# Performance work log

Hardware: AMD Instinct MI355X
Metric: run time of the kernel (lower is better)

Reference implementation:

```python
import jax, jax.numpy as jnp
import numpy as np

D_MODEL = 128; N_HEADS = 8; N_LEVELS = 1; N_POINTS = 8
MAX_RES = 10.0
B, H_SP, W_SP = 8, 64, 64


def setup_inputs() -> dict:
    key = jax.random.key(0)
    ks = jax.random.split(key, 8)
    s = 0.02
    f32 = jnp.float32
    return {
        "nbr_fea": jax.random.normal(ks[0], (B, D_MODEL, H_SP, W_SP), f32),
        "ext_fea": jax.random.normal(ks[1], (B, D_MODEL, H_SP, W_SP), f32),
        "W_val": jax.random.normal(ks[2], (D_MODEL, D_MODEL), f32) * s,
        "b_val": jnp.zeros((D_MODEL,), f32),
        "W_off": jax.random.normal(ks[3], (D_MODEL, N_HEADS * N_LEVELS * N_POINTS * 2), f32) * s,
        "b_off": jax.random.normal(ks[4], (N_HEADS * N_LEVELS * N_POINTS * 2,), f32) * s,
        "W_attn": jax.random.normal(ks[5], (D_MODEL, N_HEADS * N_LEVELS * N_POINTS), f32) * s,
        "b_attn": jnp.zeros((N_HEADS * N_LEVELS * N_POINTS,), f32),
        "W_out": jax.random.normal(ks[6], (D_MODEL, D_MODEL), f32) * s,
        "b_out": jnp.zeros((D_MODEL,), f32),
    }


def _deform_attn_align(nbr_fea, ext_fea, W_val, b_val, W_off, b_off, W_attn, b_attn, W_out, b_out):
    b, c, h, w = nbr_fea.shape
    L = h * w
    dh = c // N_HEADS
    # flatten b c h w -> b (h w) c
    query = jnp.transpose(ext_fea, (0, 2, 3, 1)).reshape(b, L, c)
    vin = jnp.transpose(nbr_fea, (0, 2, 3, 1)).reshape(b, L, c)

    # value projection (mask is all-False -> no masked fill needed)
    value = (vin @ W_val + b_val).reshape(b, L, N_HEADS, dh)
    vh = jnp.transpose(value, (0, 2, 1, 3))  # [b, H, L, dh]

    # sampling offsets, clamped by max_residue_magnitude * tanh
    off = MAX_RES * jnp.tanh(query @ W_off + b_off)
    off = off.reshape(b, L, N_HEADS, N_POINTS, 2)  # single level
    attn = jax.nn.softmax((query @ W_attn + b_attn).reshape(b, L, N_HEADS, N_POINTS), axis=-1)

    # reference points in [0,1]; valid_ratio == 1 since padding mask is all-False
    yy, xx = jnp.meshgrid(jnp.arange(h, dtype=jnp.float32), jnp.arange(w, dtype=jnp.float32), indexing="ij")
    ref = jnp.stack([(xx.reshape(-1) + 0.5) / w, (yy.reshape(-1) + 0.5) / h], axis=-1)  # [L, 2]
    norm = jnp.array([w, h], jnp.float32)  # offset_normalizer [W, H]
    loc = ref[None, :, None, None, :] + off / norm  # [b, L, H, P, 2]

    # grid_sample(align_corners=False, padding_mode='zeros') pixel coordinates
    px = jnp.transpose(loc[..., 0] * w - 0.5, (0, 2, 1, 3))  # [b, H, L, P]
    py = jnp.transpose(loc[..., 1] * h - 0.5, (0, 2, 1, 3))

    x0 = jnp.floor(px); y0 = jnp.floor(py)
    fx = px - x0; fy = py - y0
    x0i = x0.astype(jnp.int32); y0i = y0.astype(jnp.int32)

    def gather(xi, yi):
        valid = (xi >= 0) & (xi < w) & (yi >= 0) & (yi < h)
        idx = jnp.clip(yi, 0, h - 1) * w + jnp.clip(xi, 0, w - 1)  # [b, H, L, P]
        g = jnp.take_along_axis(vh, idx.reshape(b, N_HEADS, L * N_POINTS)[..., None], axis=2)
        return g.reshape(b, N_HEADS, L, N_POINTS, dh) * valid[..., None]

    samp = (gather(x0i, y0i) * ((1.0 - fx) * (1.0 - fy))[..., None]
            + gather(x0i + 1, y0i) * (fx * (1.0 - fy))[..., None]
            + gather(x0i, y0i + 1) * ((1.0 - fx) * fy)[..., None]
            + gather(x0i + 1, y0i + 1) * (fx * fy)[..., None])  # [b, H, L, P, dh]

    aw = jnp.transpose(attn, (0, 2, 1, 3))  # [b, H, L, P]
    out = jnp.sum(samp * aw[..., None], axis=3)  # [b, H, L, dh]
    out = jnp.transpose(out, (0, 2, 1, 3)).reshape(b, L, c)
    out = out @ W_out + b_out
    return jnp.transpose(out.reshape(b, h, w, c), (0, 3, 1, 2))  # b c h w


def reference(nbr_fea, ext_fea, W_val, b_val, W_off, b_off, W_attn, b_attn, W_out, b_out):
    return _deform_attn_align(nbr_fea, ext_fea, W_val, b_val, W_off, b_off, W_attn, b_attn, W_out, b_out)
```

## Files before the change

kernel.cpp:

```cpp
#include <hip/hip_runtime.h>
#include <cstdint>

#define HB 8
#define CM 128
#define NHEAD 8
#define NPT 8
#define DHD 16
#define HS 64
#define WS 64
#define LTOT 4096
#define NQA 192

typedef float floatx4 __attribute__((ext_vector_type(4)));
typedef short bf16x8 __attribute__((ext_vector_type(8)));

__device__ __forceinline__ unsigned short f2bf_rne(float x) {
  unsigned u = __float_as_uint(x);
  return (unsigned short)((u + 0x7FFFu + ((u >> 16) & 1)) >> 16);
}
__device__ __forceinline__ void split_bf(float x, unsigned short& h, unsigned short& l) {
  unsigned u = __float_as_uint(x);
  h = (unsigned short)(u >> 16);
  float r = x - __uint_as_float(u & 0xFFFF0000u);
  l = (unsigned short)(__float_as_uint(r) >> 16);
}
__device__ __forceinline__ float fast_tanh(float x) {
  float e = __expf(2.0f * x);
  return 1.0f - 2.0f / (e + 1.0f);
}

__global__ __launch_bounds__(256) void prep(const float* __restrict__ Wv,
                                            const float* __restrict__ Wo,
                                            const float* __restrict__ Wa,
                                            const float* __restrict__ Ww,
                                            const float* __restrict__ bo,
                                            const float* __restrict__ ba,
                                            unsigned short* __restrict__ wf_val,
                                            unsigned short* __restrict__ wf_qa,
                                            unsigned short* __restrict__ wf_out,
                                            float* __restrict__ bias_qa) {
  const int gid = blockIdx.x * 256 + threadIdx.x;
  const int k4 = gid / 448;
  const int ng = gid - k4 * 448;

  const float* src;
  unsigned short* dst;
  int Nsrc, Nn, nd, n;
  if (ng < 128) {        src = Wv; dst = wf_val; Nsrc = 128; Nn = 128; n = ng;        nd = n; }
  else if (ng < 256) {   src = Wo; dst = wf_qa;  Nsrc = 128; Nn = 192; n = ng - 128;  nd = n; }
  else if (ng < 320) {   src = Wa; dst = wf_qa;  Nsrc = 64;  Nn = 192; n = ng - 256;  nd = n + 128; }
  else {                 src = Ww; dst = wf_out; Nsrc = 128; Nn = 128; n = ng - 320;  nd = n; }

  ushort4 hi, lo;
  split_bf(src[(k4 * 4 + 0) * Nsrc + n], hi.x, lo.x);
  split_bf(src[(k4 * 4 + 1) * Nsrc + n], hi.y, lo.y);
  split_bf(src[(k4 * 4 + 2) * Nsrc + n], hi.z, lo.z);
  split_bf(src[(k4 * 4 + 3) * Nsrc + n], hi.w, lo.w);
  const int off = (k4 >> 1) * Nn * 8 + nd * 8 + (k4 & 1) * 4;
  *(ushort4*)(dst + off) = hi;
  *(ushort4*)(dst + Nn * 128 + off) = lo;

  if (gid < 128) bias_qa[gid] = bo[gid];
  else if (gid < 192) bias_qa[gid] = ba[gid - 128];
}

template <int N, int OUT_MODE>
__device__ __forceinline__ void gemm_wide(const float* __restrict__ A,
                                          const unsigned short* __restrict__ WF,
                                          const float* __restrict__ bias,
                                          void* __restrict__ outv,
                                          int b, int ml0, int t, char* smem) {
  constexpr int NT = N / 32;
  unsigned short* AB = (unsigned short*)smem;

  {
    const float* src = A + (size_t)b * CM * LTOT + ml0;
    const int x = t & 63, kq = t >> 6;
#pragma unroll
    for (int i = 0; i < 8; i++) {
      const int kb = kq * 4 + i * 16;
      ushort4 hi, lo;
      split_bf(src[(size_t)(kb + 0) * LTOT + x], hi.x, lo.x);
      split_bf(src[(size_t)(kb + 1) * LTOT + x], hi.y, lo.y);
      split_bf(src[(size_t)(kb + 2) * LTOT + x], hi.z, lo.z);
      split_bf(src[(size_t)(kb + 3) * LTOT + x], hi.w, lo.w);
      const int off = x * 128 + (((kb >> 3) ^ (x & 15)) << 3) + (kb & 7);
      *(ushort4*)(AB + off) = hi;
      *(ushort4*)(AB + 8192 + off) = lo;
    }
  }
  __syncthreads();

  const int w = t >> 6, lane = t & 63;
  const int wm = (w >> 1) * 32, wn = (w & 1) * (N / 2);
  const int nl = lane & 15, q = lane >> 4;

  floatx4 acc[2][NT];
#pragma unroll
  for (int mt = 0; mt < 2; mt++)
#pragma unroll
    for (int j = 0; j < NT; j++) acc[mt][j] = {0.0f, 0.0f, 0.0f, 0.0f};

#pragma unroll
  for (int K0 = 0; K0 < 4; K0++) {
    bf16x8 ah[2], al[2];
#pragma unroll
    for (int mt = 0; mt < 2; mt++) {
      const int m = wm + mt * 16 + nl;
      const int off = m * 128 + (((K0 * 4 + q) ^ (m & 15)) << 3);
      ah[mt] = *(bf16x8*)(AB + off);
      al[mt] = *(bf16x8*)(AB + 8192 + off);
    }
#pragma unroll
    for (int j = 0; j < NT; j++) {
      const int n = wn + j * 16 + nl;
      const size_t o = (size_t)(K0 * 4 + q) * N * 8 + n * 8;
      const bf16x8 wh = *(const bf16x8*)(WF + o);
      const bf16x8 wl = *(const bf16x8*)(WF + (size_t)N * 128 + o);
#pragma unroll
      for (int mt = 0; mt < 2; mt++) {
        acc[mt][j] = __builtin_amdgcn_mfma_f32_16x16x32_bf16(al[mt], wh, acc[mt][j], 0, 0, 0);
        acc[mt][j] = __builtin_amdgcn_mfma_f32_16x16x32_bf16(ah[mt], wl, acc[mt][j], 0, 0, 0);
        acc[mt][j] = __builtin_amdgcn_mfma_f32_16x16x32_bf16(ah[mt], wh, acc[mt][j], 0, 0, 0);
      }
    }
  }

#pragma unroll
  for (int j = 0; j < NT; j++) {
    const int gc = wn + j * 16 + nl;
    const float bv = bias[gc];
#pragma unroll
    for (int mt = 0; mt < 2; mt++)
#pragma unroll
      for (int r = 0; r < 4; r++) {
        const int m = ml0 + wm + mt * 16 + q * 4 + r;
        const float v = acc[mt][j][r] + bv;
        if (OUT_MODE == 0)
          ((unsigned short*)outv)[(((size_t)b * NHEAD + (gc >> 4)) * LTOT + m) * DHD + (gc & 15)] =
              f2bf_rne(v);
        else
          ((float*)outv)[((size_t)b * LTOT + m) * NQA + gc] = v;
      }
  }
}

__global__ __launch_bounds__(256, 4) void gemm_vq(const float* __restrict__ nbr,
                                                  const float* __restrict__ ext,
                                                  const unsigned short* __restrict__ wf_val,
                                                  const unsigned short* __restrict__ wf_qa,
                                                  const float* __restrict__ b_val,
                                                  const float* __restrict__ bias_qa,
                                                  unsigned short* __restrict__ value,
                                                  float* __restrict__ qa) {
  __shared__ char smem[32768];
  if (blockIdx.y == 0)
    gemm_wide<128, 0>(nbr, wf_val, b_val, value, blockIdx.z, blockIdx.x * 64, threadIdx.x, smem);
  else
    gemm_wide<192, 1>(ext, wf_qa, bias_qa, qa, blockIdx.z, blockIdx.x * 64, threadIdx.x, smem);
}

__global__ __launch_bounds__(512, 2) void samp_out(const unsigned short* __restrict__ value,
                                                   const float* __restrict__ qa,
                                                   const unsigned short* __restrict__ wf_out,
                                                   const float* __restrict__ b_out,
                                                   float* __restrict__ out) {
  __shared__ char smem[65536];
  float2* WXY = (float2*)smem;
  float* WA = (float*)(smem + 32768);
  unsigned short* FR = (unsigned short*)(smem + 49152);
  const int t = threadIdx.x;
  const int b = blockIdx.x & 7;
  const int tile = blockIdx.x >> 3;
  const int ml0 = tile * 64;

  {
    const int ll = t >> 3, h = t & 7;
    const int l = ml0 + ll;
    const float* qrow = qa + ((size_t)b * LTOT + l) * NQA;
    float4 of[4];
#pragma unroll
    for (int j = 0; j < 4; j++) of[j] = *(const float4*)(qrow + h * 16 + j * 4);
    const float4 lga = *(const float4*)(qrow + 128 + h * 8);
    const float4 lgb = *(const float4*)(qrow + 128 + h * 8 + 4);
    const float lg[8] = {lga.x, lga.y, lga.z, lga.w, lgb.x, lgb.y, lgb.z, lgb.w};
    float m = lg[0];
#pragma unroll
    for (int p = 1; p < 8; p++) m = fmaxf(m, lg[p]);
    float e[8], s = 0.0f;
#pragma unroll
    for (int p = 0; p < 8; p++) { e[p] = __expf(lg[p] - m); s += e[p]; }
    const float inv = 1.0f / s;
    const float xf = (float)(l & (WS - 1));
    const float yf = (float)(l >> 6);
#pragma unroll
    for (int p = 0; p < 8; p++) {
      const float ox = (p & 1) ? of[p >> 1].z : of[p >> 1].x;
      const float oy = (p & 1) ? of[p >> 1].w : of[p >> 1].y;
      WXY[p * 512 + t] = {xf + 10.0f * fast_tanh(ox), yf + 10.0f * fast_tanh(oy)};
      WA[p * 512 + t] = e[p] * inv;
    }
  }
  __syncthreads();

  const int d4 = t & 3;
  const int u = t >> 2;
#pragma unroll
  for (int ps = 0; ps < 4; ps++) {
    const int uu = ps * 128 + u;
    const int ll = uu >> 3;
    const int h = uu & 7;
    const unsigned short* vbb = value + ((size_t)(b * NHEAD + h) * LTOT) * DHD + d4 * 4;

    float4 o = {0.0f, 0.0f, 0.0f, 0.0f};
#pragma unroll
    for (int p = 0; p < 8; p++) {
      const float2 pxy = WXY[p * 512 + uu];
      const float aw = WA[p * 512 + uu];
      const float x0f = floorf(pxy.x), y0f = floorf(pxy.y);
      const float fx = pxy.x - x0f, fy = pxy.y - y0f;
      const int ix = (int)x0f, iy = (int)y0f;
#pragma unroll
      for (int c = 0; c < 4; c++) {
        const int cdx = c & 1, cdy = c >> 1;
        const int jx = ix + cdx, jy = iy + cdy;
        const float wx = cdx ? fx : 1.0f - fx;
        const float wy = cdy ? fy : 1.0f - fy;
        const bool valid = ((unsigned)jx < WS) & ((unsigned)jy < HS);
        const float wc = valid ? aw * wx * wy : 0.0f;
        const int cx = min(max(jx, 0), WS - 1);
        const int cy = min(max(jy, 0), HS - 1);
        const uint2 rw = *(const uint2*)(vbb + (size_t)((cy << 6) + cx) * DHD);
        o.x += wc * __uint_as_float(rw.x << 16);
        o.y += wc * __uint_as_float(rw.x & 0xFFFF0000u);
        o.z += wc * __uint_as_float(rw.y << 16);
        o.w += wc * __uint_as_float(rw.y & 0xFFFF0000u);
      }
    }

    const int off = ll * 128 + (((h * 2 + (d4 >> 1)) ^ (ll & 15)) << 3) + (d4 & 1) * 4;
    ushort4 st = {f2bf_rne(o.x), f2bf_rne(o.y), f2bf_rne(o.z), f2bf_rne(o.w)};
    *(ushort4*)(FR + off) = st;
  }
  __syncthreads();

  const int w = t >> 6, lane = t & 63;
  const int nl = lane & 15, q = lane >> 4;
  const int wm = (w >> 1) * 16;
  const int wn = (w & 1) * 64;

  floatx4 acc[4];
#pragma unroll
  for (int j = 0; j < 4; j++) acc[j] = {0.0f, 0.0f, 0.0f, 0.0f};

#pragma unroll
  for (int K0 = 0; K0 < 4; K0++) {
    const int m = wm + nl;
    const int off = m * 128 + (((K0 * 4 + q) ^ (m & 15)) << 3);
    const bf16x8 ah = *(bf16x8*)(FR + off);
#pragma unroll
    for (int j = 0; j < 4; j++) {
      const int n = wn + j * 16 + nl;
      const size_t o = (size_t)(K0 * 4 + q) * CM * 8 + n * 8;
      const bf16x8 wh = *(const bf16x8*)(wf_out + o);
      const bf16x8 wl = *(const bf16x8*)(wf_out + (size_t)CM * 128 + o);
      acc[j] = __builtin_amdgcn_mfma_f32_16x16x32_bf16(ah, wl, acc[j], 0, 0, 0);
      acc[j] = __builtin_amdgcn_mfma_f32_16x16x32_bf16(ah, wh, acc[j], 0, 0, 0);
    }
  }

  __syncthreads();
  float* LF = (float*)smem;
#pragma unroll
  for (int j = 0; j < 4; j++) {
    const int n = wn + j * 16 + nl;
#pragma unroll
    for (int r = 0; r < 4; r++) LF[n * 65 + wm + q * 4 + r] = acc[j][r];
  }
  __syncthreads();

#pragma unroll
  for (int i = 0; i < 16; i++) {
    const int idx = t + i * 512;
    const int n = idx >> 6, m = idx & 63;
    out[((size_t)b * CM + n) * LTOT + ml0 + m] = LF[n * 65 + m] + b_out[n];
  }
}

extern "C" void kernel_launch(void* const* d_in, const int* in_sizes, int n_in,
                              void* d_out, int out_size, void* d_ws, size_t ws_size,
                              hipStream_t stream) {
  const float* nbr    = (const float*)d_in[0];
  const float* ext    = (const float*)d_in[1];
  const float* W_val  = (const float*)d_in[2];
  const float* b_val  = (const float*)d_in[3];
  const float* W_off  = (const float*)d_in[4];
  const float* b_off  = (const float*)d_in[5];
  const float* W_attn = (const float*)d_in[6];
  const float* b_attn = (const float*)d_in[7];
  const float* W_out  = (const float*)d_in[8];
  const float* b_out  = (const float*)d_in[9];
  float* out = (float*)d_out;

  unsigned short* value = (unsigned short*)d_ws;
  float* qa = (float*)(value + (size_t)HB * NHEAD * LTOT * DHD);
  unsigned short* wf_val = (unsigned short*)(qa + (size_t)HB * LTOT * NQA);
  unsigned short* wf_qa  = wf_val + 128 * 128 * 2;
  unsigned short* wf_out = wf_qa + 192 * 128 * 2;
  float* bias_qa = (float*)(wf_out + 128 * 128 * 2);

  prep<<<56, 256, 0, stream>>>(W_val, W_off, W_attn, W_out, b_off, b_attn,
                               wf_val, wf_qa, wf_out, bias_qa);
  gemm_vq<<<dim3(64, 2, HB), 256, 0, stream>>>(nbr, ext, wf_val, wf_qa, b_val, bias_qa, value, qa);
  samp_out<<<dim3(512), 512, 0, stream>>>(value, qa, wf_out, b_out, out);
}
```

Measured before the change: 136.1 us.

## Fuse projection GEMMs, sampling and output GEMM into one persistent kernel with grid barrier

Merges the value/query GEMM kernel and the sampling+output kernel into a single 512-block kernel. Each block computes its value-projection tile, publishes it via an atomic counter, then computes the offset/attention projection straight into shared memory, so the qa intermediate never goes to global memory. It then spins on a grid-wide barrier before sampling value. This drops one kernel launch and the qa round-trip, but relies on all 512 blocks being co-resident to avoid deadlock and adds a spin-wait.

```diff
diff --git a/kernel.cpp b/kernel.cpp
--- a/kernel.cpp
+++ b/kernel.cpp
@@ -10,6 +10,8 @@
 #define WS 64
 #define LTOT 4096
 #define NQA 192
+#define QAP 196
+#define NBLK 512
 
 typedef float floatx4 __attribute__((ext_vector_type(4)));
 typedef short bf16x8 __attribute__((ext_vector_type(8)));
@@ -38,8 +40,10 @@
                                             unsigned short* __restrict__ wf_val,
                                             unsigned short* __restrict__ wf_qa,
                                             unsigned short* __restrict__ wf_out,
-                                            float* __restrict__ bias_qa) {
+                                            float* __restrict__ bias_qa,
+                                            unsigned int* __restrict__ bar) {
   const int gid = blockIdx.x * 256 + threadIdx.x;
+  if (gid == 0) *bar = 0;
   const int k4 = gid / 448;
   const int ng = gid - k4 * 448;
 
@@ -64,21 +68,37 @@
   else if (gid < 192) bias_qa[gid] = ba[gid - 128];
 }
 
-template <int N, int OUT_MODE>
-__device__ __forceinline__ void gemm_wide(const float* __restrict__ A,
-                                          const unsigned short* __restrict__ WF,
-                                          const float* __restrict__ bias,
-                                          void* __restrict__ outv,
-                                          int b, int ml0, int t, char* smem) {
-  constexpr int NT = N / 32;
+__global__ __launch_bounds__(512, 4) void fused(const float* __restrict__ nbr,
+                                                const float* __restrict__ ext,
+                                                const unsigned short* __restrict__ wf_val,
+                                                const unsigned short* __restrict__ wf_qa,
+                                                const unsigned short* __restrict__ wf_out,
+                                                const float* __restrict__ b_val,
+                                                const float* __restrict__ bias_qa,
+                                                const float* __restrict__ b_out,
+                                                unsigned short* __restrict__ value,
+                                                float* __restrict__ out,
+                                                unsigned int* __restrict__ bar) {
+  __shared__ char smem[65536];
   unsigned short* AB = (unsigned short*)smem;
-
-  {
-    const float* src = A + (size_t)b * CM * LTOT + ml0;
+  float* qaT = (float*)smem;
+  float2* WXY = (float2*)smem;
+  float* WA = (float*)(smem + 32768);
+  unsigned short* FR = (unsigned short*)(smem + 49152);
+  float* LF = (float*)smem;
+
+  const int t = threadIdx.x;
+  const int b = blockIdx.x & 7;
+  const int ml0 = (blockIdx.x >> 3) * 64;
+  const int wv = t >> 6, lane = t & 63;
+  const int nl = lane & 15, q = lane >> 4;
+
+  {
+    const float* src = nbr + (size_t)b * CM * LTOT + ml0;
     const int x = t & 63, kq = t >> 6;
 #pragma unroll
-    for (int i = 0; i < 8; i++) {
-      const int kb = kq * 4 + i * 16;
+    for (int i = 0; i < 4; i++) {
+      const int kb = i * 32 + kq * 4;
       ushort4 hi, lo;
       split_bf(src[(size_t)(kb + 0) * LTOT + x], hi.x, lo.x);
       split_bf(src[(size_t)(kb + 1) * LTOT + x], hi.y, lo.y);
@@ -91,98 +111,118 @@
   }
   __syncthreads();
 
-  const int w = t >> 6, lane = t & 63;
-  const int wm = (w >> 1) * 32, wn = (w & 1) * (N / 2);
-  const int nl = lane & 15, q = lane >> 4;
-
-  floatx4 acc[2][NT];
-#pragma unroll
-  for (int mt = 0; mt < 2; mt++)
-#pragma unroll
-    for (int j = 0; j < NT; j++) acc[mt][j] = {0.0f, 0.0f, 0.0f, 0.0f};
-
-#pragma unroll
-  for (int K0 = 0; K0 < 4; K0++) {
-    bf16x8 ah[2], al[2];
-#pragma unroll
-    for (int mt = 0; mt < 2; mt++) {
-      const int m = wm + mt * 16 + nl;
-      const int off = m * 128 + (((K0 * 4 + q) ^ (m & 15)) << 3);
-      ah[mt] = *(bf16x8*)(AB + off);
-      al[mt] = *(bf16x8*)(AB + 8192 + off);
-    }
-#pragma unroll
-    for (int j = 0; j < NT; j++) {
+  {
+    const int wn = wv * 16;
+    floatx4 acc[4];
+#pragma unroll
+    for (int mt = 0; mt < 4; mt++) acc[mt] = {0.0f, 0.0f, 0.0f, 0.0f};
+#pragma unroll
+    for (int K0 = 0; K0 < 4; K0++) {
+      bf16x8 ah[4], al[4];
+#pragma unroll
+      for (int mt = 0; mt < 4; mt++) {
+        const int off = (mt * 16 + nl) * 128 + (((K0 * 4 + q) ^ nl) << 3);
+        ah[mt] = *(bf16x8*)(AB + off);
+        al[mt] = *(bf16x8*)(AB + 8192 + off);
+      }
+      const size_t o = (size_t)(K0 * 4 + q) * CM * 8 + (wn + nl) * 8;
+      const bf16x8 wh = *(const bf16x8*)(wf_val + o);
+      const bf16x8 wl = *(const bf16x8*)(wf_val + (size_t)CM * 128 + o);
+#pragma unroll
+      for (int mt = 0; mt < 4; mt++) {
+        acc[mt] = __builtin_amdgcn_mfma_f32_16x16x32_bf16(al[mt], wh, acc[mt], 0, 0, 0);
+        acc[mt] = __builtin_amdgcn_mfma_f32_16x16x32_bf16(ah[mt], wl, acc[mt], 0, 0, 0);
+        acc[mt] = __builtin_amdgcn_mfma_f32_16x16x32_bf16(ah[mt], wh, acc[mt], 0, 0, 0);
+      }
+    }
+    const float bv = b_val[wn + nl];
+    unsigned short* vp = value + ((size_t)(b * NHEAD + wv) * LTOT) * DHD + nl;
+#pragma unroll
+    for (int mt = 0; mt < 4; mt++)
+#pragma unroll
+      for (int r = 0; r < 4; r++) {
+        const int m = ml0 + mt * 16 + q * 4 + r;
+        vp[(size_t)m * DHD] = f2bf_rne(acc[mt][r] + bv);
+      }
+  }
+  __syncthreads();
+
+  if (t == 0) {
+    __threadfence();
+    __hip_atomic_fetch_add(bar, 1u, __ATOMIC_RELEASE, __HIP_MEMORY_SCOPE_AGENT);
+  }
+
+  {
+    const float* src = ext + (size_t)b * CM * LTOT + ml0;
+    const int x = t & 63, kq = t >> 6;
+#pragma unroll
+    for (int i = 0; i < 4; i++) {
+      const int kb = i * 32 + kq * 4;
+      ushort4 hi, lo;
+      split_bf(src[(size_t)(kb + 0) * LTOT + x], hi.x, lo.x);
+      split_bf(src[(size_t)(kb + 1) * LTOT + x], hi.y, lo.y);
+      split_bf(src[(size_t)(kb + 2) * LTOT + x], hi.z, lo.z);
+      split_bf(src[(size_t)(kb + 3) * LTOT + x], hi.w, lo.w);
+      const int off = x * 128 + (((kb >> 3) ^ (x & 15)) << 3) + (kb & 7);
+      *(ushort4*)(AB + off) = hi;
+      *(ushort4*)(AB + 8192 + off) = lo;
+    }
+  }
+  __syncthreads();
+
+  {
+    const int wm = (wv >> 2) * 32;
+    const int wn = (wv & 3) * 48;
+    floatx4 acc[2][3];
+#pragma unroll
+    for (int mt = 0; mt < 2; mt++)
+#pragma unroll
+      for (int j = 0; j < 3; j++) acc[mt][j] = {0.0f, 0.0f, 0.0f, 0.0f};
+#pragma unroll
+    for (int K0 = 0; K0 < 4; K0++) {
+      bf16x8 ah[2], al[2];
+#pragma unroll
+      for (int mt = 0; mt < 2; mt++) {
+        const int off = (wm + mt * 16 + nl) * 128 + (((K0 * 4 + q) ^ nl) << 3);
+        ah[mt] = *(bf16x8*)(AB + off);
+        al[mt] = *(bf16x8*)(AB + 8192 + off);
+      }
+#pragma unroll
+      for (int j = 0; j < 3; j++) {
+        const size_t o = (size_t)(K0 * 4 + q) * NQA * 8 + (wn + j * 16 + nl) * 8;
+        const bf16x8 wh = *(const bf16x8*)(wf_qa + o);
+        const bf16x8 wl = *(const bf16x8*)(wf_qa + (size_t)NQA * 128 + o);
+#pragma unroll
+        for (int mt = 0; mt < 2; mt++) {
+          acc[mt][j] = __builtin_amdgcn_mfma_f32_16x16x32_bf16(al[mt], wh, acc[mt][j], 0, 0, 0);
+          acc[mt][j] = __builtin_amdgcn_mfma_f32_16x16x32_bf16(ah[mt], wl, acc[mt][j], 0, 0, 0);
+          acc[mt][j] = __builtin_amdgcn_mfma_f32_16x16x32_bf16(ah[mt], wh, acc[mt][j], 0, 0, 0);
+        }
+      }
+    }
+    __syncthreads();
+#pragma unroll
+    for (int j = 0; j < 3; j++) {
       const int n = wn + j * 16 + nl;
-      const size_t o = (size_t)(K0 * 4 + q) * N * 8 + n * 8;
-      const bf16x8 wh = *(const bf16x8*)(WF + o);
-      const bf16x8 wl = *(const bf16x8*)(WF + (size_t)N * 128 + o);
-#pragma unroll
-      for (int mt = 0; mt < 2; mt++) {
-        acc[mt][j] = __builtin_amdgcn_mfma_f32_16x16x32_bf16(al[mt], wh, acc[mt][j], 0, 0, 0);
-        acc[mt][j] = __builtin_amdgcn_mfma_f32_16x16x32_bf16(ah[mt], wl, acc[mt][j], 0, 0, 0);
-        acc[mt][j] = __builtin_amdgcn_mfma_f32_16x16x32_bf16(ah[mt], wh, acc[mt][j], 0, 0, 0);
-      }
-    }
-  }
-
-#pragma unroll
-  for (int j = 0; j < NT; j++) {
-    const int gc = wn + j * 16 + nl;
-    const float bv = bias[gc];
-#pragma unroll
-    for (int mt = 0; mt < 2; mt++)
-#pragma unroll
-      for (int r = 0; r < 4; r++) {
-        const int m = ml0 + wm + mt * 16 + q * 4 + r;
-        const float v = acc[mt][j][r] + bv;
-        if (OUT_MODE == 0)
-          ((unsigned short*)outv)[(((size_t)b * NHEAD + (gc >> 4)) * LTOT + m) * DHD + (gc & 15)] =
-              f2bf_rne(v);
-        else
-          ((float*)outv)[((size_t)b * LTOT + m) * NQA + gc] = v;
-      }
-  }
-}
-
-__global__ __launch_bounds__(256, 4) void gemm_vq(const float* __restrict__ nbr,
-                                                  const float* __restrict__ ext,
-                                                  const unsigned short* __restrict__ wf_val,
-                                                  const unsigned short* __restrict__ wf_qa,
-                                                  const float* __restrict__ b_val,
-                                                  const float* __restrict__ bias_qa,
-                                                  unsigned short* __restrict__ value,
-                                                  float* __restrict__ qa) {
-  __shared__ char smem[32768];
-  if (blockIdx.y == 0)
-    gemm_wide<128, 0>(nbr, wf_val, b_val, value, blockIdx.z, blockIdx.x * 64, threadIdx.x, smem);
-  else
-    gemm_wide<192, 1>(ext, wf_qa, bias_qa, qa, blockIdx.z, blockIdx.x * 64, threadIdx.x, smem);
-}
-
-__global__ __launch_bounds__(512, 2) void samp_out(const unsigned short* __restrict__ value,
-                                                   const float* __restrict__ qa,
-                                                   const unsigned short* __restrict__ wf_out,
-                                                   const float* __restrict__ b_out,
-                                                   float* __restrict__ out) {
-  __shared__ char smem[65536];
-  float2* WXY = (float2*)smem;
-  float* WA = (float*)(smem + 32768);
-  unsigned short* FR = (unsigned short*)(smem + 49152);
-  const int t = threadIdx.x;
-  const int b = blockIdx.x & 7;
-  const int tile = blockIdx.x >> 3;
-  const int ml0 = tile * 64;
+      const float bv = bias_qa[n];
+#pragma unroll
+      for (int mt = 0; mt < 2; mt++)
+#pragma unroll
+        for (int r = 0; r < 4; r++)
+          qaT[(wm + mt * 16 + q * 4 + r) * QAP + n] = acc[mt][j][r] + bv;
+    }
+  }
+  __syncthreads();
 
   {
     const int ll = t >> 3, h = t & 7;
-    const int l = ml0 + ll;
-    const float* qrow = qa + ((size_t)b * LTOT + l) * NQA;
+    const float* qrow = qaT + ll * QAP;
     float4 of[4];
 #pragma unroll
     for (int j = 0; j < 4; j++) of[j] = *(const float4*)(qrow + h * 16 + j * 4);
     const float4 lga = *(const float4*)(qrow + 128 + h * 8);
     const float4 lgb = *(const float4*)(qrow + 128 + h * 8 + 4);
+    __syncthreads();
     const float lg[8] = {lga.x, lga.y, lga.z, lga.w, lgb.x, lgb.y, lgb.z, lgb.w};
     float m = lg[0];
 #pragma unroll
@@ -191,6 +231,7 @@
 #pragma unroll
     for (int p = 0; p < 8; p++) { e[p] = __expf(lg[p] - m); s += e[p]; }
     const float inv = 1.0f / s;
+    const int l = ml0 + ll;
     const float xf = (float)(l & (WS - 1));
     const float yf = (float)(l >> 6);
 #pragma unroll
@@ -201,89 +242,91 @@
       WA[p * 512 + t] = e[p] * inv;
     }
   }
-  __syncthreads();
-
-  const int d4 = t & 3;
-  const int u = t >> 2;
-#pragma unroll
-  for (int ps = 0; ps < 4; ps++) {
-    const int uu = ps * 128 + u;
-    const int ll = uu >> 3;
-    const int h = uu & 7;
-    const unsigned short* vbb = value + ((size_t)(b * NHEAD + h) * LTOT) * DHD + d4 * 4;
-
-    float4 o = {0.0f, 0.0f, 0.0f, 0.0f};
-#pragma unroll
-    for (int p = 0; p < 8; p++) {
-      const float2 pxy = WXY[p * 512 + uu];
-      const float aw = WA[p * 512 + uu];
-      const float x0f = floorf(pxy.x), y0f = floorf(pxy.y);
-      const float fx = pxy.x - x0f, fy = pxy.y - y0f;
-      const int ix = (int)x0f, iy = (int)y0f;
-#pragma unroll
-      for (int c = 0; c < 4; c++) {
-        const int cdx = c & 1, cdy = c >> 1;
-        const int jx = ix + cdx, jy = iy + cdy;
-        const float wx = cdx ? fx : 1.0f - fx;
-        const float wy = cdy ? fy : 1.0f - fy;
-        const bool valid = ((unsigned)jx < WS) & ((unsigned)jy < HS);
-        const float wc = valid ? aw * wx * wy : 0.0f;
-        const int cx = min(max(jx, 0), WS - 1);
-        const int cy = min(max(jy, 0), HS - 1);
-        const uint2 rw = *(const uint2*)(vbb + (size_t)((cy << 6) + cx) * DHD);
-        o.x += wc * __uint_as_float(rw.x << 16);
-        o.y += wc * __uint_as_float(rw.x & 0xFFFF0000u);
-        o.z += wc * __uint_as_float(rw.y << 16);
-        o.w += wc * __uint_as_float(rw.y & 0xFFFF0000u);
-      }
-    }
-
-    const int off = ll * 128 + (((h * 2 + (d4 >> 1)) ^ (ll & 15)) << 3) + (d4 & 1) * 4;
-    ushort4 st = {f2bf_rne(o.x), f2bf_rne(o.y), f2bf_rne(o.z), f2bf_rne(o.w)};
-    *(ushort4*)(FR + off) = st;
-  }
-  __syncthreads();
-
-  const int w = t >> 6, lane = t & 63;
-  const int nl = lane & 15, q = lane >> 4;
-  const int wm = (w >> 1) * 16;
-  const int wn = (w & 1) * 64;
-
-  floatx4 acc[4];
-#pragma unroll
-  for (int j = 0; j < 4; j++) acc[j] = {0.0f, 0.0f, 0.0f, 0.0f};
-
-#pragma unroll
-  for (int K0 = 0; K0 < 4; K0++) {
-    const int m = wm + nl;
-    const int off = m * 128 + (((K0 * 4 + q) ^ (m & 15)) << 3);
-    const bf16x8 ah = *(bf16x8*)(FR + off);
+
+  if (t == 0) {
+    while (__hip_atomic_load(bar, __ATOMIC_ACQUIRE, __HIP_MEMORY_SCOPE_AGENT) < NBLK)
+      __builtin_amdgcn_s_sleep(2);
+    __threadfence();
+  }
+  __syncthreads();
+
+  {
+    const int d4 = t & 3;
+    const int u = t >> 2;
+#pragma unroll
+    for (int ps = 0; ps < 4; ps++) {
+      const int uu = ps * 128 + u;
+      const int ll = uu >> 3;
+      const int h = uu & 7;
+      const unsigned short* vbb = value + ((size_t)(b * NHEAD + h) * LTOT) * DHD + d4 * 4;
+
+      float4 o = {0.0f, 0.0f, 0.0f, 0.0f};
+#pragma unroll
+      for (int p = 0; p < 8; p++) {
+        const float2 pxy = WXY[p * 512 + uu];
+        const float aw = WA[p * 512 + uu];
+        const float x0f = floorf(pxy.x), y0f = floorf(pxy.y);
+        const float fx = pxy.x - x0f, fy = pxy.y - y0f;
+        const int ix = (int)x0f, iy = (int)y0f;
+#pragma unroll
+        for (int c = 0; c < 4; c++) {
+          const int cdx = c & 1, cdy = c >> 1;
+          const int jx = ix + cdx, jy = iy + cdy;
+          const float wx = cdx ? fx : 1.0f - fx;
+          const float wy = cdy ? fy : 1.0f - fy;
+          const bool valid = ((unsigned)jx < WS) & ((unsigned)jy < HS);
+          const float wc = valid ? aw * wx * wy : 0.0f;
+          const int cx = min(max(jx, 0), WS - 1);
+          const int cy = min(max(jy, 0), HS - 1);
+          const uint2 rw = *(const uint2*)(vbb + (size_t)((cy << 6) + cx) * DHD);
+          o.x += wc * __uint_as_float(rw.x << 16);
+          o.y += wc * __uint_as_float(rw.x & 0xFFFF0000u);
+          o.z += wc * __uint_as_float(rw.y << 16);
+          o.w += wc * __uint_as_float(rw.y & 0xFFFF0000u);
+        }
+      }
+      const int off = ll * 128 + (((h * 2 + (d4 >> 1)) ^ (ll & 15)) << 3) + (d4 & 1) * 4;
+      ushort4 st = {f2bf_rne(o.x), f2bf_rne(o.y), f2bf_rne(o.z), f2bf_rne(o.w)};
+      *(ushort4*)(FR + off) = st;
+    }
+  }
+  __syncthreads();
+
+  {
+    const int wm = (wv >> 1) * 16;
+    const int wn = (wv & 1) * 64;
+    floatx4 acc[4];
+#pragma unroll
+    for (int j = 0; j < 4; j++) acc[j] = {0.0f, 0.0f, 0.0f, 0.0f};
+#pragma unroll
+    for (int K0 = 0; K0 < 4; K0++) {
+      const int m = wm + nl;
+      const int off = m * 128 + (((K0 * 4 + q) ^ (m & 15)) << 3);
+      const bf16x8 ah = *(bf16x8*)(FR + off);
+#pragma unroll
+      for (int j = 0; j < 4; j++) {
+        const int n = wn + j * 16 + nl;
+        const size_t o = (size_t)(K0 * 4 + q) * CM * 8 + n * 8;
+        const bf16x8 wh = *(const bf16x8*)(wf_out + o);
+        const bf16x8 wl = *(const bf16x8*)(wf_out + (size_t)CM * 128 + o);
+        acc[j] = __builtin_amdgcn_mfma_f32_16x16x32_bf16(ah, wl, acc[j], 0, 0, 0);
+        acc[j] = __builtin_amdgcn_mfma_f32_16x16x32_bf16(ah, wh, acc[j], 0, 0, 0);
+      }
+    }
+    __syncthreads();
 #pragma unroll
     for (int j = 0; j < 4; j++) {
       const int n = wn + j * 16 + nl;
-      const size_t o = (size_t)(K0 * 4 + q) * CM * 8 + n * 8;
-      const bf16x8 wh = *(const bf16x8*)(wf_out + o);
-      const bf16x8 wl = *(const bf16x8*)(wf_out + (size_t)CM * 128 + o);
-      acc[j] = __builtin_amdgcn_mfma_f32_16x16x32_bf16(ah, wl, acc[j], 0, 0, 0);
-      acc[j] = __builtin_amdgcn_mfma_f32_16x16x32_bf16(ah, wh, acc[j], 0, 0, 0);
-    }
-  }
-
-  __syncthreads();
-  float* LF = (float*)smem;
-#pragma unroll
-  for (int j = 0; j < 4; j++) {
-    const int n = wn + j * 16 + nl;
-#pragma unroll
-    for (int r = 0; r < 4; r++) LF[n * 65 + wm + q * 4 + r] = acc[j][r];
-  }
-  __syncthreads();
-
-#pragma unroll
-  for (int i = 0; i < 16; i++) {
-    const int idx = t + i * 512;
-    const int n = idx >> 6, m = idx & 63;
-    out[((size_t)b * CM + n) * LTOT + ml0 + m] = LF[n * 65 + m] + b_out[n];
+#pragma unroll
+      for (int r = 0; r < 4; r++) LF[n * 65 + wm + q * 4 + r] = acc[j][r];
+    }
+    __syncthreads();
+#pragma unroll
+    for (int i = 0; i < 16; i++) {
+      const int idx = t + i * 512;
+      const int n = idx >> 6, m = idx & 63;
+      out[((size_t)b * CM + n) * LTOT + ml0 + m] = LF[n * 65 + m] + b_out[n];
+    }
   }
 }
 
@@ -303,14 +346,14 @@
   float* out = (float*)d_out;
 
   unsigned short* value = (unsigned short*)d_ws;
-  float* qa = (float*)(value + (size_t)HB * NHEAD * LTOT * DHD);
-  unsigned short* wf_val = (unsigned short*)(qa + (size_t)HB * LTOT * NQA);
+  unsigned short* wf_val = value + (size_t)HB * NHEAD * LTOT * DHD;
   unsigned short* wf_qa  = wf_val + 128 * 128 * 2;
   unsigned short* wf_out = wf_qa + 192 * 128 * 2;
   float* bias_qa = (float*)(wf_out + 128 * 128 * 2);
+  unsigned int* bar = (unsigned int*)(bias_qa + 256);
 
   prep<<<56, 256, 0, stream>>>(W_val, W_off, W_attn, W_out, b_off, b_attn,
-                               wf_val, wf_qa, wf_out, bias_qa);
-  gemm_vq<<<dim3(64, 2, HB), 256, 0, stream>>>(nbr, ext, wf_val, wf_qa, b_val, bias_qa, value, qa);
-  samp_out<<<dim3(512), 512, 0, stream>>>(value, qa, wf_out, b_out, out);
-}
+                               wf_val, wf_qa, wf_out, bias_qa, bar);
+  fused<<<dim3(NBLK), 512, 0, stream>>>(nbr, ext, wf_val, wf_qa, wf_out,
+                                        b_val, bias_qa, b_out, value, out, bar);
+}
```

After: 170.3 us. 1.25x slower.

## Fuse query offset/attention GEMM into sampling kernel, drop qa workspace roundtrip

Applied to the files above, without the earlier changes.

Moves the query projection (offsets and attention logits) out of the first GEMM kernel and into the sampling kernel, so each block computes its own 32-row qa tile in shared memory instead of writing and rereading a 192-float-per-pixel buffer in global memory. The sampling kernel now uses 256-thread blocks over 32-pixel tiles with a smaller shared footprint. The output projection stores float4 directly rather than transposing through shared memory. The cost is less parallel overlap between the value GEMM and the qa GEMM, plus extra per-block work in the sampling kernel.

```diff
diff --git a/kernel.cpp b/kernel.cpp
--- a/kernel.cpp
+++ b/kernel.cpp
@@ -10,6 +10,7 @@
 #define WS 64
 #define LTOT 4096
 #define NQA 192
+#define QAP 196
 
 typedef float floatx4 __attribute__((ext_vector_type(4)));
 typedef short bf16x8 __attribute__((ext_vector_type(8)));
@@ -64,17 +65,18 @@
   else if (gid < 192) bias_qa[gid] = ba[gid - 128];
 }
 
-template <int N, int OUT_MODE>
-__device__ __forceinline__ void gemm_wide(const float* __restrict__ A,
-                                          const unsigned short* __restrict__ WF,
-                                          const float* __restrict__ bias,
-                                          void* __restrict__ outv,
-                                          int b, int ml0, int t, char* smem) {
-  constexpr int NT = N / 32;
+__global__ __launch_bounds__(256, 4) void gemm_val(const float* __restrict__ nbr,
+                                                   const unsigned short* __restrict__ WF,
+                                                   const float* __restrict__ bias,
+                                                   unsigned short* __restrict__ value) {
+  __shared__ char smem[32768];
   unsigned short* AB = (unsigned short*)smem;
-
-  {
-    const float* src = A + (size_t)b * CM * LTOT + ml0;
+  const int t = threadIdx.x;
+  const int ml0 = blockIdx.x * 64;
+  const int b = blockIdx.y;
+
+  {
+    const float* src = nbr + (size_t)b * CM * LTOT + ml0;
     const int x = t & 63, kq = t >> 6;
 #pragma unroll
     for (int i = 0; i < 8; i++) {
@@ -92,14 +94,14 @@
   __syncthreads();
 
   const int w = t >> 6, lane = t & 63;
-  const int wm = (w >> 1) * 32, wn = (w & 1) * (N / 2);
+  const int wm = (w >> 1) * 32, wn = (w & 1) * 64;
   const int nl = lane & 15, q = lane >> 4;
 
-  floatx4 acc[2][NT];
+  floatx4 acc[2][4];
 #pragma unroll
   for (int mt = 0; mt < 2; mt++)
 #pragma unroll
-    for (int j = 0; j < NT; j++) acc[mt][j] = {0.0f, 0.0f, 0.0f, 0.0f};
+    for (int j = 0; j < 4; j++) acc[mt][j] = {0.0f, 0.0f, 0.0f, 0.0f};
 
 #pragma unroll
   for (int K0 = 0; K0 < 4; K0++) {
@@ -112,11 +114,10 @@
       al[mt] = *(bf16x8*)(AB + 8192 + off);
     }
 #pragma unroll
-    for (int j = 0; j < NT; j++) {
-      const int n = wn + j * 16 + nl;
-      const size_t o = (size_t)(K0 * 4 + q) * N * 8 + n * 8;
+    for (int j = 0; j < 4; j++) {
+      const size_t o = (size_t)(K0 * 4 + q) * CM * 8 + (wn + j * 16 + nl) * 8;
       const bf16x8 wh = *(const bf16x8*)(WF + o);
-      const bf16x8 wl = *(const bf16x8*)(WF + (size_t)N * 128 + o);
+      const bf16x8 wl = *(const bf16x8*)(WF + (size_t)CM * 128 + o);
 #pragma unroll
       for (int mt = 0; mt < 2; mt++) {
         acc[mt][j] = __builtin_amdgcn_mfma_f32_16x16x32_bf16(al[mt], wh, acc[mt][j], 0, 0, 0);
@@ -127,62 +128,100 @@
   }
 
 #pragma unroll
-  for (int j = 0; j < NT; j++) {
+  for (int j = 0; j < 4; j++) {
     const int gc = wn + j * 16 + nl;
     const float bv = bias[gc];
+    unsigned short* vp = value + ((size_t)(b * NHEAD + (gc >> 4)) * LTOT) * DHD + (gc & 15);
 #pragma unroll
     for (int mt = 0; mt < 2; mt++)
 #pragma unroll
       for (int r = 0; r < 4; r++) {
         const int m = ml0 + wm + mt * 16 + q * 4 + r;
-        const float v = acc[mt][j][r] + bv;
-        if (OUT_MODE == 0)
-          ((unsigned short*)outv)[(((size_t)b * NHEAD + (gc >> 4)) * LTOT + m) * DHD + (gc & 15)] =
-              f2bf_rne(v);
-        else
-          ((float*)outv)[((size_t)b * LTOT + m) * NQA + gc] = v;
-      }
-  }
-}
-
-__global__ __launch_bounds__(256, 4) void gemm_vq(const float* __restrict__ nbr,
-                                                  const float* __restrict__ ext,
-                                                  const unsigned short* __restrict__ wf_val,
-                                                  const unsigned short* __restrict__ wf_qa,
-                                                  const float* __restrict__ b_val,
-                                                  const float* __restrict__ bias_qa,
-                                                  unsigned short* __restrict__ value,
-                                                  float* __restrict__ qa) {
-  __shared__ char smem[32768];
-  if (blockIdx.y == 0)
-    gemm_wide<128, 0>(nbr, wf_val, b_val, value, blockIdx.z, blockIdx.x * 64, threadIdx.x, smem);
-  else
-    gemm_wide<192, 1>(ext, wf_qa, bias_qa, qa, blockIdx.z, blockIdx.x * 64, threadIdx.x, smem);
-}
-
-__global__ __launch_bounds__(512, 2) void samp_out(const unsigned short* __restrict__ value,
-                                                   const float* __restrict__ qa,
-                                                   const unsigned short* __restrict__ wf_out,
-                                                   const float* __restrict__ b_out,
-                                                   float* __restrict__ out) {
-  __shared__ char smem[65536];
+        vp[(size_t)m * DHD] = f2bf_rne(acc[mt][j][r] + bv);
+      }
+  }
+}
+
+__global__ __launch_bounds__(256, 3) void samp(const float* __restrict__ ext,
+                                               const unsigned short* __restrict__ value,
+                                               const unsigned short* __restrict__ wf_qa,
+                                               const unsigned short* __restrict__ wf_out,
+                                               const float* __restrict__ bias_qa,
+                                               const float* __restrict__ b_out,
+                                               float* __restrict__ out) {
+  __shared__ char smem[41472];
+  unsigned short* AB = (unsigned short*)smem;
+  float* qaT = (float*)(smem + 16384);
   float2* WXY = (float2*)smem;
-  float* WA = (float*)(smem + 32768);
-  unsigned short* FR = (unsigned short*)(smem + 49152);
+  float* WA = (float*)(smem + 16384);
+  unsigned short* FR = (unsigned short*)(smem + 24576);
+
   const int t = threadIdx.x;
   const int b = blockIdx.x & 7;
-  const int tile = blockIdx.x >> 3;
-  const int ml0 = tile * 64;
+  const int ml0 = (blockIdx.x >> 3) * 32;
+  const int w = t >> 6, lane = t & 63;
+  const int nl = lane & 15, q = lane >> 4;
+
+  {
+    const float* src = ext + (size_t)b * CM * LTOT + ml0;
+    const int x = t & 31, kq = t >> 5;
+#pragma unroll
+    for (int i = 0; i < 4; i++) {
+      const int kb = i * 32 + kq * 4;
+      ushort4 hi, lo;
+      split_bf(src[(size_t)(kb + 0) * LTOT + x], hi.x, lo.x);
+      split_bf(src[(size_t)(kb + 1) * LTOT + x], hi.y, lo.y);
+      split_bf(src[(size_t)(kb + 2) * LTOT + x], hi.z, lo.z);
+      split_bf(src[(size_t)(kb + 3) * LTOT + x], hi.w, lo.w);
+      const int off = x * 128 + (((kb >> 3) ^ (x & 15)) << 3) + (kb & 7);
+      *(ushort4*)(AB + off) = hi;
+      *(ushort4*)(AB + 4096 + off) = lo;
+    }
+  }
+  __syncthreads();
+
+  {
+    const int wm = (w & 1) * 16;
+    const int wn = (w >> 1) * 96;
+    floatx4 acc[6];
+#pragma unroll
+    for (int j = 0; j < 6; j++) acc[j] = {0.0f, 0.0f, 0.0f, 0.0f};
+#pragma unroll
+    for (int K0 = 0; K0 < 4; K0++) {
+      const int m = wm + nl;
+      const int off = m * 128 + (((K0 * 4 + q) ^ (m & 15)) << 3);
+      const bf16x8 ah = *(bf16x8*)(AB + off);
+      const bf16x8 al = *(bf16x8*)(AB + 4096 + off);
+#pragma unroll
+      for (int j = 0; j < 6; j++) {
+        const size_t o = (size_t)(K0 * 4 + q) * NQA * 8 + (wn + j * 16 + nl) * 8;
+        const bf16x8 wh = *(const bf16x8*)(wf_qa + o);
+        const bf16x8 wl = *(const bf16x8*)(wf_qa + (size_t)NQA * 128 + o);
+        acc[j] = __builtin_amdgcn_mfma_f32_16x16x32_bf16(al, wh, acc[j], 0, 0, 0);
+        acc[j] = __builtin_amdgcn_mfma_f32_16x16x32_bf16(ah, wl, acc[j], 0, 0, 0);
+        acc[j] = __builtin_amdgcn_mfma_f32_16x16x32_bf16(ah, wh, acc[j], 0, 0, 0);
+      }
+    }
+#pragma unroll
+    for (int j = 0; j < 6; j++) {
+      const int n = wn + j * 16 + nl;
+      const float bv = bias_qa[n];
+#pragma unroll
+      for (int r = 0; r < 4; r++)
+        qaT[(wm + q * 4 + r) * QAP + n] = acc[j][r] + bv;
+    }
+  }
+  __syncthreads();
 
   {
     const int ll = t >> 3, h = t & 7;
-    const int l = ml0 + ll;
-    const float* qrow = qa + ((size_t)b * LTOT + l) * NQA;
+    const float* qrow = qaT + ll * QAP;
     float4 of[4];
 #pragma unroll
     for (int j = 0; j < 4; j++) of[j] = *(const float4*)(qrow + h * 16 + j * 4);
     const float4 lga = *(const float4*)(qrow + 128 + h * 8);
     const float4 lgb = *(const float4*)(qrow + 128 + h * 8 + 4);
+    __syncthreads();
     const float lg[8] = {lga.x, lga.y, lga.z, lga.w, lgb.x, lgb.y, lgb.z, lgb.w};
     float m = lg[0];
 #pragma unroll
@@ -191,99 +230,89 @@
 #pragma unroll
     for (int p = 0; p < 8; p++) { e[p] = __expf(lg[p] - m); s += e[p]; }
     const float inv = 1.0f / s;
+    const int l = ml0 + ll;
     const float xf = (float)(l & (WS - 1));
     const float yf = (float)(l >> 6);
 #pragma unroll
     for (int p = 0; p < 8; p++) {
       const float ox = (p & 1) ? of[p >> 1].z : of[p >> 1].x;
       const float oy = (p & 1) ? of[p >> 1].w : of[p >> 1].y;
-      WXY[p * 512 + t] = {xf + 10.0f * fast_tanh(ox), yf + 10.0f * fast_tanh(oy)};
-      WA[p * 512 + t] = e[p] * inv;
-    }
-  }
-  __syncthreads();
-
-  const int d4 = t & 3;
-  const int u = t >> 2;
-#pragma unroll
-  for (int ps = 0; ps < 4; ps++) {
-    const int uu = ps * 128 + u;
-    const int ll = uu >> 3;
-    const int h = uu & 7;
-    const unsigned short* vbb = value + ((size_t)(b * NHEAD + h) * LTOT) * DHD + d4 * 4;
-
-    float4 o = {0.0f, 0.0f, 0.0f, 0.0f};
-#pragma unroll
-    for (int p = 0; p < 8; p++) {
-      const float2 pxy = WXY[p * 512 + uu];
-      const float aw = WA[p * 512 + uu];
-      const float x0f = floorf(pxy.x), y0f = floorf(pxy.y);
-      const float fx = pxy.x - x0f, fy = pxy.y - y0f;
-      const int ix = (int)x0f, iy = (int)y0f;
-#pragma unroll
-      for (int c = 0; c < 4; c++) {
-        const int cdx = c & 1, cdy = c >> 1;
-        const int jx = ix + cdx, jy = iy + cdy;
-        const float wx = cdx ? fx : 1.0f - fx;
-        const float wy = cdy ? fy : 1.0f - fy;
-        const bool valid = ((unsigned)jx < WS) & ((unsigned)jy < HS);
-        const float wc = valid ? aw * wx * wy : 0.0f;
-        const int cx = min(max(jx, 0), WS - 1);
-        const int cy = min(max(jy, 0), HS - 1);
-        const uint2 rw = *(const uint2*)(vbb + (size_t)((cy << 6) + cx) * DHD);
-        o.x += wc * __uint_as_float(rw.x << 16);
-        o.y += wc * __uint_as_float(rw.x & 0xFFFF0000u);
-        o.z += wc * __uint_as_float(rw.y << 16);
-        o.w += wc * __uint_as_float(rw.y & 0xFFFF0000u);
-      }
-    }
-
-    const int off = ll * 128 + (((h * 2 + (d4 >> 1)) ^ (ll & 15)) << 3) + (d4 & 1) * 4;
-    ushort4 st = {f2bf_rne(o.x), f2bf_rne(o.y), f2bf_rne(o.z), f2bf_rne(o.w)};
-    *(ushort4*)(FR + off) = st;
-  }
-  __syncthreads();
-
-  const int w = t >> 6, lane = t & 63;
-  const int nl = lane & 15, q = lane >> 4;
-  const int wm = (w >> 1) * 16;
-  const int wn = (w & 1) * 64;
-
-  floatx4 acc[4];
-#pragma unroll
-  for (int j = 0; j < 4; j++) acc[j] = {0.0f, 0.0f, 0.0f, 0.0f};
-
-#pragma unroll
-  for (int K0 = 0; K0 < 4; K0++) {
-    const int m = wm + nl;
-    const int off = m * 128 + (((K0 * 4 + q) ^ (m & 15)) << 3);
-    const bf16x8 ah = *(bf16x8*)(FR + off);
+      WXY[p * 256 + t] = {xf + 10.0f * fast_tanh(ox), yf + 10.0f * fast_tanh(oy)};
+      WA[p * 256 + t] = e[p] * inv;
+    }
+  }
+  __syncthreads();
+
+  {
+    const int d4 = t & 3;
+    const int u = t >> 2;
+#pragma unroll
+    for (int ps = 0; ps < 4; ps++) {
+      const int uu = ps * 64 + u;
+      const int ll = uu >> 3;
+      const int h = uu & 7;
+      const unsigned short* vbb = value + ((size_t)(b * NHEAD + h) * LTOT) * DHD + d4 * 4;
+
+      float4 o = {0.0f, 0.0f, 0.0f, 0.0f};
+#pragma unroll
+      for (int p = 0; p < 8; p++) {
+        const float2 pxy = WXY[p * 256 + uu];
+        const float aw = WA[p * 256 + uu];
+        const float x0f = floorf(pxy.x), y0f = floorf(pxy.y);
+        const float fx = pxy.x - x0f, fy = pxy.y - y0f;
+        const int ix = (int)x0f, iy = (int)y0f;
+#pragma unroll
+        for (int c = 0; c < 4; c++) {
+          const int cdx = c & 1, cdy = c >> 1;
+          const int jx = ix + cdx, jy = iy + cdy;
+          const float wx = cdx ? fx : 1.0f - fx;
+          const float wy = cdy ? fy : 1.0f - fy;
+          const bool valid = ((unsigned)jx < WS) & ((unsigned)jy < HS);
+          const float wc = valid ? aw * wx * wy : 0.0f;
+          const int cx = min(max(jx, 0), WS - 1);
+          const int cy = min(max(jy, 0), HS - 1);
+          const uint2 rw = *(const uint2*)(vbb + (size_t)((cy << 6) + cx) * DHD);
+          o.x += wc * __uint_as_float(rw.x << 16);
+          o.y += wc * __uint_as_float(rw.x & 0xFFFF0000u);
+          o.z += wc * __uint_as_float(rw.y << 16);
+          o.w += wc * __uint_as_float(rw.y & 0xFFFF0000u);
+        }
+      }
+      const int off = ll * 128 + (((h * 2 + (d4 >> 1)) ^ (ll & 15)) << 3) + (d4 & 1) * 4;
+      ushort4 st = {f2bf_rne(o.x), f2bf_rne(o.y), f2bf_rne(o.z), f2bf_rne(o.w)};
+      *(ushort4*)(FR + off) = st;
+    }
+  }
+  __syncthreads();
+
+  {
+    const int wm = (w & 1) * 16;
+    const int wn = (w >> 1) * 64;
+    floatx4 acc[4];
+#pragma unroll
+    for (int j = 0; j < 4; j++) acc[j] = {0.0f, 0.0f, 0.0f, 0.0f};
+#pragma unroll
+    for (int K0 = 0; K0 < 4; K0++) {
+      const int m = wm + nl;
+      const int off = m * 128 + (((K0 * 4 + q) ^ (m & 15)) << 3);
+      const bf16x8 ah = *(bf16x8*)(FR + off);
+#pragma unroll
+      for (int j = 0; j < 4; j++) {
+        const int n = wn + j * 16 + nl;
+        const size_t o = (size_t)(K0 * 4 + q) * CM * 8 + n * 8;
+        const bf16x8 wh = *(const bf16x8*)(wf_out + o);
+        const bf16x8 wl = *(const bf16x8*)(wf_out + (size_t)CM * 128 + o);
+        acc[j] = __builtin_amdgcn_mfma_f32_16x16x32_bf16(ah, wl, acc[j], 0, 0, 0);
+        acc[j] = __builtin_amdgcn_mfma_f32_16x16x32_bf16(ah, wh, acc[j], 0, 0, 0);
+      }
+    }
 #pragma unroll
     for (int j = 0; j < 4; j++) {
-      const int n = wn + j * 16 + nl;
-      const size_t o = (size_t)(K0 * 4 + q) * CM * 8 + n * 8;
-      const bf16x8 wh = *(const bf16x8*)(wf_out + o);
-      const bf16x8 wl = *(const bf16x8*)(wf_out + (size_t)CM * 128 + o);
-      acc[j] = __builtin_amdgcn_mfma_f32_16x16x32_bf16(ah, wl, acc[j], 0, 0, 0);
-      acc[j] = __builtin_amdgcn_mfma_f32_16x16x32_bf16(ah, wh, acc[j], 0, 0, 0);
-    }
-  }
-
-  __syncthreads();
-  float* LF = (float*)smem;
-#pragma unroll
-  for (int j = 0; j < 4; j++) {
-    const int n = wn + j * 16 + nl;
-#pragma unroll
-    for (int r = 0; r < 4; r++) LF[n * 65 + wm + q * 4 + r] = acc[j][r];
-  }
-  __syncthreads();
-
-#pragma unroll
-  for (int i = 0; i < 16; i++) {
-    const int idx = t + i * 512;
-    const int n = idx >> 6, m = idx & 63;
-    out[((size_t)b * CM + n) * LTOT + ml0 + m] = LF[n * 65 + m] + b_out[n];
+      const int gc = wn + j * 16 + nl;
+      const float bv = b_out[gc];
+      float4 st = {acc[j][0] + bv, acc[j][1] + bv, acc[j][2] + bv, acc[j][3] + bv};
+      *(float4*)(out + ((size_t)b * CM + gc) * LTOT + ml0 + wm + q * 4) = st;
+    }
   }
 }
 
@@ -303,14 +332,13 @@
   float* out = (float*)d_out;
 
   unsigned short* value = (unsigned short*)d_ws;
-  float* qa = (float*)(value + (size_t)HB * NHEAD * LTOT * DHD);
-  unsigned short* wf_val = (unsigned short*)(qa + (size_t)HB * LTOT * NQA);
+  unsigned short* wf_val = value + (size_t)HB * NHEAD * LTOT * DHD;
   unsigned short* wf_qa  = wf_val + 128 * 128 * 2;
   unsigned short* wf_out = wf_qa + 192 * 128 * 2;
   float* bias_qa = (float*)(wf_out + 128 * 128 * 2);
 
   prep<<<56, 256, 0, stream>>>(W_val, W_off, W_attn, W_out, b_off, b_attn,
                                wf_val, wf_qa, wf_out, bias_qa);
-  gemm_vq<<<dim3(64, 2, HB), 256, 0, stream>>>(nbr, ext, wf_val, wf_qa, b_val, bias_qa, value, qa);
-  samp_out<<<dim3(512), 512, 0, stream>>>(value, qa, wf_out, b_out, out);
-}
+  gemm_val<<<dim3(64, HB), 256, 0, stream>>>(nbr, wf_val, b_val, value);
+  samp<<<dim3(128 * HB), 256, 0, stream>>>(ext, value, wf_qa, wf_out, bias_qa, b_out, out);
+}
```

Measured after the change: 142.1 us. 1.04x slower.
